# Performance work log

Measured on AMD Instinct MI355X. Metric: run time of the kernel, lower is better.

The kernel has to match this reference:

```python
import jax, jax.numpy as jnp
import numpy as np

B, T, D, H, C = 128, 256, 512, 1024, 1000
FORGET_BIAS = 1.0  # tf BasicLSTMCell default


def setup_inputs() -> dict:
    key = jax.random.key(0)
    k0, k1, k2, k3 = jax.random.split(key, 4)
    x = jax.random.normal(k0, (B, T, D), dtype=jnp.float32)
    # BasicLSTMCell kernel: [D+H, 4H] (gate order i, j, f, o); bias zero-init in TF
    Wk = jax.random.normal(k1, (D + H, 4 * H), dtype=jnp.float32) * 0.01
    bk = jnp.zeros((4 * H,), dtype=jnp.float32)
    # Output projection (truncated_normal(0, 0.01) in source; plain normal ok for reference)
    w = jax.random.normal(k2, (H, C), dtype=jnp.float32) * 0.01
    b = jax.random.normal(k3, (C,), dtype=jnp.float32) * 0.01
    return {"x": x, "Wk": Wk, "bk": bk, "w": w, "b": b}


def reference(x, Wk, bk, w, b):
    Bq, Tq, Dq = x.shape
    Hq = w.shape[0]

    def step(carry, xt):
        h, c = carry
        z = jnp.concatenate([xt, h], axis=-1) @ Wk + bk  # [B, 4H]
        i, j, f, o = jnp.split(z, 4, axis=-1)            # gate order i, j, f, o
        c_new = c * jax.nn.sigmoid(f + FORGET_BIAS) + jax.nn.sigmoid(i) * jnp.tanh(j)
        h_new = jax.nn.sigmoid(o) * jnp.tanh(c_new)
        return (h_new, c_new), None

    h0 = jnp.zeros((Bq, Hq), dtype=x.dtype)
    c0 = jnp.zeros((Bq, Hq), dtype=x.dtype)
    (hT, _), _ = jax.lax.scan(step, (h0, c0), jnp.swapaxes(x, 0, 1))  # scan over T
    return hT @ w + b  # [B, C]
```

## Files before the change

kernel.cpp:

```cpp
#include <hip/hip_runtime.h>
#include <math.h>

#define B 128
#define T 256
#define D 512
#define H 1024
#define KTOT 1536
#define N4 4096

#define HSTRIDE ((size_t)B * H + 2048)

typedef short short8 __attribute__((ext_vector_type(8)));
typedef float f32x16 __attribute__((ext_vector_type(16)));

__device__ __forceinline__ unsigned short f2bf(float f) {
    unsigned int u = __builtin_bit_cast(unsigned int, f);
    unsigned int r = (u + 0x7fffu + ((u >> 16) & 1u)) >> 16;
    return (unsigned short)r;
}
__device__ __forceinline__ float bf2f(unsigned short s) {
    unsigned int u = ((unsigned int)s) << 16;
    return __builtin_bit_cast(float, u);
}
__device__ __forceinline__ float sigm(float x) { return 1.f / (1.f + __expf(-x)); }
__device__ __forceinline__ float tanh_fast(float x) {
    return 1.f - 2.f / (1.f + __expf(2.f * x));
}

__global__ __launch_bounds__(256) void convert_x(
    const float* __restrict__ x, unsigned short* __restrict__ xb)
{
    int bid = blockIdx.x;
    int t = bid >> 7;
    int b = bid & 127;
    int d = threadIdx.x * 2;
    const float2 v = *(const float2*)&x[((size_t)b * T + t) * D + d];
    unsigned int packed = (unsigned int)f2bf(v.x) | ((unsigned int)f2bf(v.y) << 16);
    *(unsigned int*)&xb[((size_t)t * B + b) * D + d] = packed;
}

__global__ __launch_bounds__(256) void convert_W(
    const float* __restrict__ Wk, unsigned short* __restrict__ Wp)
{
    __shared__ float tile[32][33];
    int nb = blockIdx.x;
    int kb = blockIdx.y;
    int tx = threadIdx.x & 31;
    int ty = threadIdx.x >> 5;
    #pragma unroll
    for (int i = 0; i < 4; ++i) {
        int k = kb * 32 + ty + i * 8;
        tile[ty + i * 8][tx] = Wk[(size_t)k * N4 + nb * 32 + tx];
    }
    __syncthreads();
    #pragma unroll
    for (int i = 0; i < 4; ++i) {
        int n = nb * 32 + ty + i * 8;
        int pcol = ((n & 1023) << 2) | (n >> 10);
        Wp[(size_t)pcol * KTOT + kb * 32 + tx] = f2bf(tile[tx][ty + i * 8]);
    }
}

__global__ __launch_bounds__(256, 1) void lstm_persist(
    const unsigned short* __restrict__ xb,
    const unsigned short* __restrict__ Wp,
    const float* __restrict__ bk,
    unsigned short* __restrict__ hring,
    unsigned int* __restrict__ arr)
{
    __shared__ float zbuf[4][64][36];
    __shared__ unsigned short hbuf[32][20];
    __shared__ unsigned int wcnt;

    const int tid  = threadIdx.x;
    const int bi   = blockIdx.x;
    const int rg   = (bi & 7) >> 1;
    const int cg   = ((bi >> 3) << 1) | (bi & 1);
    const int kq   = tid >> 6;
    const int lane = tid & 63;
    const int l31  = lane & 31;
    const int lhi  = lane >> 5;

    const int row = rg * 32 + l31;

    if (tid == 0) wcnt = 0;

    short8 wb[48];
    const unsigned short* wb0 = Wp + (size_t)(cg * 64 + l31) * KTOT + lhi * 8;
    const unsigned short* wb1 = wb0 + (size_t)32 * KTOT;
    #pragma unroll
    for (int j = 0; j < 8; ++j) {
        int k = (kq * 8 + j) * 16;
        wb[2 * j]     = *(const short8*)(wb0 + k);
        wb[2 * j + 1] = *(const short8*)(wb1 + k);
    }
    #pragma unroll
    for (int j = 0; j < 16; ++j) {
        int k = 512 + (kq * 16 + j) * 16;
        wb[16 + 2 * j]     = *(const short8*)(wb0 + k);
        wb[16 + 2 * j + 1] = *(const short8*)(wb1 + k);
    }

    float bi_[2], bj_[2], bf_[2], bo_[2];
    #pragma unroll
    for (int u = 0; u < 2; ++u) {
        int e   = tid + u * 256;
        int hcl = e >> 5;
        int hcg = cg * 16 + hcl;
        bi_[u] = bk[hcg];
        bj_[u] = bk[H + hcg];
        bf_[u] = bk[2 * H + hcg] + 1.0f;
        bo_[u] = bk[3 * H + hcg];
    }
    float cs0 = 0.f, cs1 = 0.f;

    const unsigned int* const fpoll = arr + (rg << 6) + (kq << 4) + (lane & 15);
    unsigned int* const fmine = arr + (rg << 6) + cg;
    const unsigned short* const xbase = xb + (size_t)row * D + kq * 128 + lhi * 8;
    const size_t hoff = (size_t)(rg * 64 + kq * 16) * 512 + l31 * 16 + lhi * 8;
    const size_t soff = (size_t)(rg * 64 + cg) * 256;

    const f32x16 fz = {0.f,0.f,0.f,0.f,0.f,0.f,0.f,0.f,
                       0.f,0.f,0.f,0.f,0.f,0.f,0.f,0.f};

    __syncthreads();

    for (int t = 0; t < T; ++t) {
        f32x16 a00 = fz, a01 = fz, a10 = fz, a11 = fz;

        const unsigned short* xr = xbase + (size_t)t * (B * D);
        short8 xv[8];
        #pragma unroll
        for (int j = 0; j < 8; ++j)
            xv[j] = *(const short8*)(xr + j * 16);

        short8 hv[16];
        const bool have_h = (t > 0);
        if (have_h) {
            while (__hip_atomic_load(fpoll, __ATOMIC_RELAXED,
                                     __HIP_MEMORY_SCOPE_AGENT) < (unsigned)t)
                __builtin_amdgcn_s_sleep(1);
            asm volatile("" ::: "memory");

            const unsigned short* hp = hring + (size_t)(t - 1) * HSTRIDE + hoff;
            #pragma unroll
            for (int j = 0; j < 16; ++j)
                hv[j] = *(const short8*)(hp + j * 512);
        }

        #pragma unroll
        for (int j = 0; j < 8; ++j) {
            if (j & 1) {
                a10 = __builtin_amdgcn_mfma_f32_32x32x16_bf16(xv[j], wb[2 * j],     a10, 0, 0, 0);
                a11 = __builtin_amdgcn_mfma_f32_32x32x16_bf16(xv[j], wb[2 * j + 1], a11, 0, 0, 0);
            } else {
                a00 = __builtin_amdgcn_mfma_f32_32x32x16_bf16(xv[j], wb[2 * j],     a00, 0, 0, 0);
                a01 = __builtin_amdgcn_mfma_f32_32x32x16_bf16(xv[j], wb[2 * j + 1], a01, 0, 0, 0);
            }
        }
        if (have_h) {
            #pragma unroll
            for (int j = 0; j < 16; ++j) {
                if (j & 1) {
                    a10 = __builtin_amdgcn_mfma_f32_32x32x16_bf16(hv[j], wb[16 + 2 * j],     a10, 0, 0, 0);
                    a11 = __builtin_amdgcn_mfma_f32_32x32x16_bf16(hv[j], wb[16 + 2 * j + 1], a11, 0, 0, 0);
                } else {
                    a00 = __builtin_amdgcn_mfma_f32_32x32x16_bf16(hv[j], wb[16 + 2 * j],     a00, 0, 0, 0);
                    a01 = __builtin_amdgcn_mfma_f32_32x32x16_bf16(hv[j], wb[16 + 2 * j + 1], a01, 0, 0, 0);
                }
            }
        }

        f32x16 z0 = a00 + a10;
        f32x16 z1 = a01 + a11;

        #pragma unroll
        for (int q = 0; q < 4; ++q) {
            float4 v0 = { z0[4 * q + 0], z0[4 * q + 1], z0[4 * q + 2], z0[4 * q + 3] };
            *(float4*)&zbuf[kq][l31][lhi * 4 + q * 8] = v0;
            float4 v1 = { z1[4 * q + 0], z1[4 * q + 1], z1[4 * q + 2], z1[4 * q + 3] };
            *(float4*)&zbuf[kq][32 + l31][lhi * 4 + q * 8] = v1;
        }
        __syncthreads();

        #pragma unroll
        for (int u = 0; u < 2; ++u) {
            int e   = tid + u * 256;
            int r   = e & 31;
            int hcl = e >> 5;
            int pcb = hcl * 4;
            float zi = zbuf[0][pcb + 0][r] + zbuf[1][pcb + 0][r]
                     + zbuf[2][pcb + 0][r] + zbuf[3][pcb + 0][r] + bi_[u];
            float zj = zbuf[0][pcb + 1][r] + zbuf[1][pcb + 1][r]
                     + zbuf[2][pcb + 1][r] + zbuf[3][pcb + 1][r] + bj_[u];
            float zf = zbuf[0][pcb + 2][r] + zbuf[1][pcb + 2][r]
                     + zbuf[2][pcb + 2][r] + zbuf[3][pcb + 2][r] + bf_[u];
            float zo = zbuf[0][pcb + 3][r] + zbuf[1][pcb + 3][r]
                     + zbuf[2][pcb + 3][r] + zbuf[3][pcb + 3][r] + bo_[u];
            float& cc = u ? cs1 : cs0;
            float cn = cc * sigm(zf) + sigm(zi) * tanh_fast(zj);
            cc = cn;
            float hn = sigm(zo) * tanh_fast(cn);
            hbuf[r][hcl] = f2bf(hn);
        }
        __syncthreads();

        {
            int r  = tid >> 3;
            int cp = tid & 7;
            unsigned int v = *(const unsigned int*)&hbuf[r][cp * 2];
            unsigned int* hdst = (unsigned int*)(hring + (size_t)t * HSTRIDE);
            __hip_atomic_store(&hdst[soff + tid], v,
                               __ATOMIC_RELAXED, __HIP_MEMORY_SCOPE_AGENT);
        }
        asm volatile("s_waitcnt vmcnt(0)" ::: "memory");
        if (lane == 0) {
            unsigned int old = __hip_atomic_fetch_add(&wcnt, 1u, __ATOMIC_RELAXED,
                                                      __HIP_MEMORY_SCOPE_WORKGROUP);
            if (old == 4u * (unsigned)t + 3u)
                __hip_atomic_store(fmine, (unsigned)(t + 1),
                                   __ATOMIC_RELAXED, __HIP_MEMORY_SCOPE_AGENT);
        }
    }
}

__global__ __launch_bounds__(256) void proj_kernel(
    const unsigned short* __restrict__ hb, const float* __restrict__ w,
    const float* __restrict__ bias, float* __restrict__ out)
{
    int cidx = blockIdx.x * 256 + threadIdx.x;
    int bg   = blockIdx.y;
    bool valid = cidx < 1000;
    float acc[16];
    #pragma unroll
    for (int i = 0; i < 16; ++i) acc[i] = 0.f;

    for (int k = 0; k < H; k += 4) {
        float w0 = 0.f, w1 = 0.f, w2 = 0.f, w3 = 0.f;
        if (valid) {
            w0 = w[(size_t)(k + 0) * 1000 + cidx];
            w1 = w[(size_t)(k + 1) * 1000 + cidx];
            w2 = w[(size_t)(k + 2) * 1000 + cidx];
            w3 = w[(size_t)(k + 3) * 1000 + cidx];
        }
        #pragma unroll
        for (int i = 0; i < 16; ++i) {
            int row = bg * 16 + i;
            size_t a = (size_t)((row >> 5) * 64 + (k >> 4)) * 512
                     + (size_t)(row & 31) * 16 + (k & 15);
            ushort4 hv = *(const ushort4*)&hb[a];
            acc[i] += bf2f(hv.x) * w0 + bf2f(hv.y) * w1
                    + bf2f(hv.z) * w2 + bf2f(hv.w) * w3;
        }
    }
    if (valid) {
        #pragma unroll
        for (int i = 0; i < 16; ++i)
            out[(size_t)(bg * 16 + i) * 1000 + cidx] = acc[i] + bias[cidx];
    }
}

extern "C" void kernel_launch(void* const* d_in, const int* in_sizes, int n_in,
                              void* d_out, int out_size, void* d_ws, size_t ws_size,
                              hipStream_t stream) {
    const float* x  = (const float*)d_in[0];
    const float* Wk = (const float*)d_in[1];
    const float* bk = (const float*)d_in[2];
    const float* w  = (const float*)d_in[3];
    const float* b  = (const float*)d_in[4];
    float* out = (float*)d_out;

    char* p = (char*)d_ws;
    unsigned short* xb = (unsigned short*)p;  p += (size_t)B * T * D * 2;
    unsigned short* Wp = (unsigned short*)p;  p += (size_t)N4 * KTOT * 2;
    unsigned short* hr = (unsigned short*)p;  p += HSTRIDE * T * 2;
    unsigned int*   ar = (unsigned int*)p;    p += 4 * 64 * 4;

    hipMemsetAsync(ar, 0, 4 * 64 * 4, stream);

    convert_x<<<dim3(T * B), dim3(256), 0, stream>>>(x, xb);
    convert_W<<<dim3(N4 / 32, KTOT / 32), dim3(256), 0, stream>>>(Wk, Wp);

    lstm_persist<<<dim3(256), dim3(256), 0, stream>>>(xb, Wp, bk, hr, ar);

    proj_kernel<<<dim3(4, 8), dim3(256), 0, stream>>>(hr + (size_t)(T - 1) * HSTRIDE,
                                                      w, b, out);
}
```

Baseline: 1.551 ms.

## Use per-wave arrival flags and progressive h loading with interleaved x MFMAs

Result: faster. 1.324 ms (-14.6%).

```diff
diff --git a/kernel.cpp b/kernel.cpp
--- a/kernel.cpp
+++ b/kernel.cpp
@@ -70,7 +70,6 @@
 {
     __shared__ float zbuf[4][64][36];
     __shared__ unsigned short hbuf[32][20];
-    __shared__ unsigned int wcnt;
 
     const int tid  = threadIdx.x;
     const int bi   = blockIdx.x;
@@ -83,8 +82,6 @@
 
     const int row = rg * 32 + l31;
 
-    if (tid == 0) wcnt = 0;
-
     short8 wb[48];
     const unsigned short* wb0 = Wp + (size_t)(cg * 64 + l31) * KTOT + lhi * 8;
     const unsigned short* wb1 = wb0 + (size_t)32 * KTOT;
@@ -114,8 +111,8 @@
     }
     float cs0 = 0.f, cs1 = 0.f;
 
-    const unsigned int* const fpoll = arr + (rg << 6) + (kq << 4) + (lane & 15);
-    unsigned int* const fmine = arr + (rg << 6) + cg;
+    const unsigned int* const fpoll = arr + rg * 256 + kq * 64 + lane;
+    unsigned int* const fmine = arr + rg * 256 + cg * 4 + kq;
     const unsigned short* const xbase = xb + (size_t)row * D + kq * 128 + lhi * 8;
     const size_t hoff = (size_t)(rg * 64 + kq * 16) * 512 + l31 * 16 + lhi * 8;
     const size_t soff = (size_t)(rg * 64 + cg) * 256;
@@ -123,8 +120,6 @@
     const f32x16 fz = {0.f,0.f,0.f,0.f,0.f,0.f,0.f,0.f,
                        0.f,0.f,0.f,0.f,0.f,0.f,0.f,0.f};
 
-    __syncthreads();
-
     for (int t = 0; t < T; ++t) {
         f32x16 a00 = fz, a01 = fz, a10 = fz, a11 = fz;
 
@@ -134,31 +129,31 @@
         for (int j = 0; j < 8; ++j)
             xv[j] = *(const short8*)(xr + j * 16);
 
-        short8 hv[16];
-        const bool have_h = (t > 0);
-        if (have_h) {
-            while (__hip_atomic_load(fpoll, __ATOMIC_RELAXED,
-                                     __HIP_MEMORY_SCOPE_AGENT) < (unsigned)t)
-                __builtin_amdgcn_s_sleep(1);
-            asm volatile("" ::: "memory");
-
+        if (t > 0) {
+            unsigned fv = __hip_atomic_load(fpoll, __ATOMIC_RELAXED,
+                                            __HIP_MEMORY_SCOPE_AGENT);
+            unsigned long long rb = __ballot(fv >= (unsigned)t);
             const unsigned short* hp = hring + (size_t)(t - 1) * HSTRIDE + hoff;
+            short8 hv[16];
             #pragma unroll
-            for (int j = 0; j < 16; ++j)
+            for (int j = 0; j < 16; ++j) {
+                while (((rb >> (4 * j)) & 0xFull) != 0xFull) {
+                    fv = __hip_atomic_load(fpoll, __ATOMIC_RELAXED,
+                                           __HIP_MEMORY_SCOPE_AGENT);
+                    rb = __ballot(fv >= (unsigned)t);
+                }
+                asm volatile("" ::: "memory");
                 hv[j] = *(const short8*)(hp + j * 512);
-        }
-
-        #pragma unroll
-        for (int j = 0; j < 8; ++j) {
-            if (j & 1) {
-                a10 = __builtin_amdgcn_mfma_f32_32x32x16_bf16(xv[j], wb[2 * j],     a10, 0, 0, 0);
-                a11 = __builtin_amdgcn_mfma_f32_32x32x16_bf16(xv[j], wb[2 * j + 1], a11, 0, 0, 0);
-            } else {
-                a00 = __builtin_amdgcn_mfma_f32_32x32x16_bf16(xv[j], wb[2 * j],     a00, 0, 0, 0);
-                a01 = __builtin_amdgcn_mfma_f32_32x32x16_bf16(xv[j], wb[2 * j + 1], a01, 0, 0, 0);
+                if (j < 8) {
+                    if (j & 1) {
+                        a10 = __builtin_amdgcn_mfma_f32_32x32x16_bf16(xv[j], wb[2 * j],     a10, 0, 0, 0);
+                        a11 = __builtin_amdgcn_mfma_f32_32x32x16_bf16(xv[j], wb[2 * j + 1], a11, 0, 0, 0);
+                    } else {
+                        a00 = __builtin_amdgcn_mfma_f32_32x32x16_bf16(xv[j], wb[2 * j],     a00, 0, 0, 0);
+                        a01 = __builtin_amdgcn_mfma_f32_32x32x16_bf16(xv[j], wb[2 * j + 1], a01, 0, 0, 0);
+                    }
+                }
             }
-        }
-        if (have_h) {
             #pragma unroll
             for (int j = 0; j < 16; ++j) {
                 if (j & 1) {
@@ -167,6 +162,17 @@
                 } else {
                     a00 = __builtin_amdgcn_mfma_f32_32x32x16_bf16(hv[j], wb[16 + 2 * j],     a00, 0, 0, 0);
                     a01 = __builtin_amdgcn_mfma_f32_32x32x16_bf16(hv[j], wb[16 + 2 * j + 1], a01, 0, 0, 0);
+                }
+            }
+        } else {
+            #pragma unroll
+            for (int j = 0; j < 8; ++j) {
+                if (j & 1) {
+                    a10 = __builtin_amdgcn_mfma_f32_32x32x16_bf16(xv[j], wb[2 * j],     a10, 0, 0, 0);
+                    a11 = __builtin_amdgcn_mfma_f32_32x32x16_bf16(xv[j], wb[2 * j + 1], a11, 0, 0, 0);
+                } else {
+                    a00 = __builtin_amdgcn_mfma_f32_32x32x16_bf16(xv[j], wb[2 * j],     a00, 0, 0, 0);
+                    a01 = __builtin_amdgcn_mfma_f32_32x32x16_bf16(xv[j], wb[2 * j + 1], a01, 0, 0, 0);
                 }
             }
         }
@@ -213,11 +219,9 @@
             __hip_atomic_store(&hdst[soff + tid], v,
                                __ATOMIC_RELAXED, __HIP_MEMORY_SCOPE_AGENT);
         }
-        asm volatile("s_waitcnt vmcnt(0)" ::: "memory");
-        if (lane == 0) {
-            unsigned int old = __hip_atomic_fetch_add(&wcnt, 1u, __ATOMIC_RELAXED,
-                                                      __HIP_MEMORY_SCOPE_WORKGROUP);
-            if (old == 4u * (unsigned)t + 3u)
+        if (t != T - 1) {
+            asm volatile("s_waitcnt vmcnt(0)" ::: "memory");
+            if (lane == 0)
                 __hip_atomic_store(fmine, (unsigned)(t + 1),
                                    __ATOMIC_RELAXED, __HIP_MEMORY_SCOPE_AGENT);
         }
@@ -274,9 +278,9 @@
     unsigned short* xb = (unsigned short*)p;  p += (size_t)B * T * D * 2;
     unsigned short* Wp = (unsigned short*)p;  p += (size_t)N4 * KTOT * 2;
     unsigned short* hr = (unsigned short*)p;  p += HSTRIDE * T * 2;
-    unsigned int*   ar = (unsigned int*)p;    p += 4 * 64 * 4;
-
-    hipMemsetAsync(ar, 0, 4 * 64 * 4, stream);
+    unsigned int*   ar = (unsigned int*)p;    p += 4 * 64 * 4 * 4;
+
+    hipMemsetAsync(ar, 0, 4 * 64 * 4 * 4, stream);
 
     convert_x<<<dim3(T * B), dim3(256), 0, stream>>>(x, xb);
     convert_W<<<dim3(N4 / 32, KTOT / 32), dim3(256), 0, stream>>>(Wk, Wp);
```
